# Performance work log

Hardware: AMD Instinct MI355X
Metric: run time of the kernel (lower is better)

The kernel has to match this reference:

```python
import jax, jax.numpy as jnp
import numpy as np

EPS = 1e-5
TOP_K = 2


def setup_inputs() -> dict:
    key = jax.random.key(0)
    ks = jax.random.split(key, 8)
    B, T, D, E, F = 4, 2048, 1024, 8, 4096
    s_in = 1.0 / np.sqrt(D)
    s_ff = 1.0 / np.sqrt(F)
    return {
        "hidden_states": jax.random.normal(ks[0], (B, T, D), jnp.float32),
        "input_tensor": jax.random.normal(ks[1], (B, T, D), jnp.float32),
        "gate_w": jax.random.normal(ks[2], (D, E), jnp.float32) * s_in,
        "gate_b": jnp.zeros((E,), jnp.float32),
        "w1": jax.random.normal(ks[3], (E, D, F), jnp.float32) * s_in,
        "b1": jnp.zeros((E, F), jnp.float32),
        "w2": jax.random.normal(ks[4], (E, F, D), jnp.float32) * s_ff,
        "b2": jnp.zeros((E, D), jnp.float32),
        "gamma": jnp.ones((D,), jnp.float32),
        "beta": jnp.zeros((D,), jnp.float32),
    }


def _layer_norm(x, gamma, beta):
    mu = jnp.mean(x, axis=-1, keepdims=True)
    var = jnp.mean(jnp.square(x - mu), axis=-1, keepdims=True)
    return (x - mu) * jax.lax.rsqrt(var + EPS) * gamma + beta


def reference(hidden_states, input_tensor, gate_w, gate_b, w1, b1, w2, b2, gamma, beta):
    E = gate_b.shape[0]
    # Router: softmax over experts, then top-k gate values/indices.
    gate_logits = jnp.einsum("btd,de->bte", hidden_states, gate_w) + gate_b
    gate_probs = jax.nn.softmax(gate_logits, axis=-1)
    topk_gates, topk_idx = jax.lax.top_k(gate_probs, TOP_K)  # [B,T,K]
    # Combine weights per expert: sum of top-k gate values routed to expert e.
    combine_w = jnp.sum(
        jax.nn.one_hot(topk_idx, E, dtype=hidden_states.dtype)
        * topk_gates[..., None],
        axis=-2,
    )  # [B,T,E]
    # Dispatch/combine: weighted sum of expert FFN outputs (loop over small fixed E).
    expert_outputs = jnp.zeros_like(hidden_states)
    for e in range(E):
        h = jax.nn.gelu(jnp.einsum("btd,df->btf", hidden_states, w1[e]) + b1[e])
        y = jnp.einsum("btf,fd->btd", h, w2[e]) + b2[e]
        expert_outputs = expert_outputs + combine_w[..., e:e + 1] * y
    # Dropout is identity in eval mode.
    return _layer_norm(expert_outputs + input_tensor, gamma, beta)
```

## Files before the change

kernel.cpp:

```cpp
#include <hip/hip_runtime.h>

#define TOKENS 8192
#define DIM 1024
#define NEXP 8
#define FDIM 4096

typedef __bf16 bf16x8 __attribute__((ext_vector_type(8)));
typedef float f32x4 __attribute__((ext_vector_type(4)));
typedef float f32x16 __attribute__((ext_vector_type(16)));

__device__ __forceinline__ unsigned short f2bf(float f) {
  unsigned u = __builtin_bit_cast(unsigned, f);
  u += 0x7fffu + ((u >> 16) & 1u);
  return (unsigned short)(u >> 16);
}

__device__ __forceinline__ float bf2f(unsigned short s) {
  unsigned u = (unsigned)s << 16;
  return __builtin_bit_cast(float, u);
}

__device__ __forceinline__ void gload16(const void* g, void* l) {
  __builtin_amdgcn_global_load_lds(
      (const __attribute__((address_space(1))) unsigned int*)g,
      (__attribute__((address_space(3))) unsigned int*)l, 16, 0, 0);
}

__device__ __forceinline__ void transpose_tile(const float* __restrict__ src,
                                               unsigned short* __restrict__ dstp,
                                               int R, int C, int bi2,
                                               void* smraw, int tid) {
  unsigned int (*lt)[64] = (unsigned int(*)[64])smraw;
  const int e = bi2 >> 9;
  const int w = bi2 & 511;
  const int nft = C >> 6;
  const int dt = w / nft, ft = w % nft;
  const int r0 = dt * 128, c0 = ft * 64;
  const float* s = src + (size_t)e * R * C;
  unsigned short* dout = dstp + (size_t)e * R * C;

#pragma unroll
  for (int pi = 0; pi < 4; ++pi) {
    const int idx = tid + pi * 256;
    const int dp = idx >> 4;
    const int f0 = (idx & 15) * 4;
    const float4 va = *(const float4*)(s + (size_t)(r0 + dp * 2) * C + c0 + f0);
    const float4 vb = *(const float4*)(s + (size_t)(r0 + dp * 2 + 1) * C + c0 + f0);
    const float a[4] = {va.x, va.y, va.z, va.w};
    const float b[4] = {vb.x, vb.y, vb.z, vb.w};
#pragma unroll
    for (int j = 0; j < 4; ++j) {
      const int f = f0 + j;
      lt[f][dp ^ (((f >> 2) & 7) << 2)] =
          (unsigned)f2bf(a[j]) | ((unsigned)f2bf(b[j]) << 16);
    }
  }
  __syncthreads();
#pragma unroll
  for (int wi = 0; wi < 4; ++wi) {
    const int idx = tid + wi * 256;
    const int f = idx >> 4;
    const int dp0 = (idx & 15) * 4;
    const int sw = ((f >> 2) & 7) << 2;
    uint4 o = *(const uint4*)&lt[f][dp0 ^ sw];
    *(uint4*)(dout + (size_t)(c0 + f) * R + r0 + dp0 * 2) = o;
  }
}

__global__ void prep_kernel(const float* __restrict__ w1,
                            unsigned short* __restrict__ w1t,
                            const float* __restrict__ hs,
                            const float* __restrict__ gw,
                            const float* __restrict__ gb,
                            int* __restrict__ counts,
                            int* __restrict__ tok_idx,
                            float* __restrict__ tok_w,
                            unsigned int* __restrict__ slotinfo,
                            unsigned short* __restrict__ hs_bf) {
  __shared__ unsigned int lt[64][64];
  const int L = blockIdx.x;

  if (L < 2048) {
    const int lane = threadIdx.x & 63;
    const int wid = threadIdx.x >> 6;
    const int t = L * 4 + wid;
    const float* row = hs + (size_t)t * DIM;

    float x[16];
    const float4* r4 = (const float4*)(row + lane * 16);
#pragma unroll
    for (int i = 0; i < 4; ++i) {
      float4 v = r4[i];
      x[i * 4 + 0] = v.x; x[i * 4 + 1] = v.y; x[i * 4 + 2] = v.z; x[i * 4 + 3] = v.w;
    }

    float acc[8];
#pragma unroll
    for (int e = 0; e < 8; ++e) acc[e] = 0.f;
#pragma unroll
    for (int i = 0; i < 16; ++i) {
      const int d = lane * 16 + i;
      const float4* g4 = (const float4*)(gw + (size_t)d * 8);
      float4 g0 = g4[0], g1 = g4[1];
      const float xv = x[i];
      acc[0] += xv * g0.x; acc[1] += xv * g0.y; acc[2] += xv * g0.z; acc[3] += xv * g0.w;
      acc[4] += xv * g1.x; acc[5] += xv * g1.y; acc[6] += xv * g1.z; acc[7] += xv * g1.w;
    }
#pragma unroll
    for (int sh = 1; sh < 64; sh <<= 1) {
#pragma unroll
      for (int e = 0; e < 8; ++e) acc[e] += __shfl_xor(acc[e], sh, 64);
    }
#pragma unroll
    for (int e = 0; e < 8; ++e) acc[e] += gb[e];

    float mx = acc[0];
#pragma unroll
    for (int e = 1; e < 8; ++e) mx = fmaxf(mx, acc[e]);
    float p[8];
    float sum = 0.f;
#pragma unroll
    for (int e = 0; e < 8; ++e) { p[e] = __expf(acc[e] - mx); sum += p[e]; }
    const float inv = 1.0f / sum;

    int i0 = 0; float b0 = p[0];
#pragma unroll
    for (int e = 1; e < 8; ++e) if (p[e] > b0) { b0 = p[e]; i0 = e; }
    int i1 = -1; float b1v = -1.f;
#pragma unroll
    for (int e = 0; e < 8; ++e) if (e != i0 && p[e] > b1v) { b1v = p[e]; i1 = e; }

    if (lane == 0) {
      int pos0 = atomicAdd(&counts[i0], 1);
      tok_idx[i0 * TOKENS + pos0] = t;
      tok_w[i0 * TOKENS + pos0] = b0 * inv;
      int pos1 = atomicAdd(&counts[i1], 1);
      tok_idx[i1 * TOKENS + pos1] = t;
      tok_w[i1 * TOKENS + pos1] = b1v * inv;
      slotinfo[t] = ((unsigned)i0 << 29) | ((unsigned)pos0 << 16) |
                    ((unsigned)i1 << 13) | (unsigned)pos1;
    }

    unsigned short us[16];
#pragma unroll
    for (int i = 0; i < 16; ++i) us[i] = f2bf(x[i]);
    uint4 o0, o1;
    o0.x = (unsigned)us[0] | ((unsigned)us[1] << 16);
    o0.y = (unsigned)us[2] | ((unsigned)us[3] << 16);
    o0.z = (unsigned)us[4] | ((unsigned)us[5] << 16);
    o0.w = (unsigned)us[6] | ((unsigned)us[7] << 16);
    o1.x = (unsigned)us[8] | ((unsigned)us[9] << 16);
    o1.y = (unsigned)us[10] | ((unsigned)us[11] << 16);
    o1.z = (unsigned)us[12] | ((unsigned)us[13] << 16);
    o1.w = (unsigned)us[14] | ((unsigned)us[15] << 16);
    uint4* dst = (uint4*)(hs_bf + (size_t)t * DIM + lane * 16);
    dst[0] = o0;
    dst[1] = o1;
    return;
  }

  transpose_tile(w1, w1t, DIM, FDIM, L - 2048, lt, threadIdx.x);
}

template<int MODE, int K, int N>
__global__ __launch_bounds__(256, 4)
void moe_gemm(const unsigned short* __restrict__ Abase,
              const unsigned short* __restrict__ Bbase,
              const float* __restrict__ bias,
              const int* __restrict__ counts,
              const int* __restrict__ tok_idx,
              unsigned short* __restrict__ dst,
              const float* __restrict__ w2src,
              unsigned short* __restrict__ w2t) {
  constexpr int NS = K / 32;
  constexpr int NQ = (MODE == 0) ? 8 : 2;
  __shared__ __align__(16) unsigned char sm[32768];

  int L = blockIdx.x;
  if (MODE == 0) {
    const int q = L / 5, r = L % 5;
    if (r >= 3) {
      transpose_tile(w2src, w2t, FDIM, DIM, q * 2 + (r - 3), sm, threadIdx.x);
      return;
    }
    L = q * 3 + r;
  }

  const int xk = L & 7;
  const int tt = L >> 3;
  const int g = (tt >> 4) * 8 + xk;
  const int within = tt & 15;

  int e = 0, mcq = 0, n4 = 0, goff = 0, cnt = 0;
  {
    int accC = 0, accOff = 0;
    bool found = false;
#pragma unroll
    for (int ee = 0; ee < NEXP; ++ee) {
      const int c = counts[ee];
      const int mt = (c + 127) >> 7;
      const int mc4 = (mt + 3) >> 2;
      const int ch = mc4 * NQ;
      if (!found && g < accC + ch) {
        const int local = g - accC;
        e = ee;
        mcq = (local / NQ) * 4;
        n4 = (local % NQ) * 4;
        goff = accOff;
        cnt = c;
        found = true;
      }
      accC += ch;
      accOff += c;
    }
    if (!found) return;
  }
  const int m0 = (mcq + (within >> 2)) * 128;
  if (m0 >= cnt) return;
  const int n0 = (n4 + (within & 3)) * 128;

  const int tid = threadIdx.x;
  const int lane = tid & 63;
  const int wid = tid >> 6;
  const int wm = wid >> 1;
  const int wn = wid & 1;
  const int l31 = lane & 31;
  const int lh = lane >> 5;

  const int trow = tid >> 2;
  const int tswz = (tid & 3) ^ ((trow >> 1) & 3) ^ ((trow >> 3) & 3);
  const unsigned char* Bexp = (const unsigned char*)(Bbase + (size_t)e * K * N);

  int gA0 = m0 + trow;      if (gA0 > cnt - 1) gA0 = cnt - 1;
  int gA1 = m0 + trow + 64; if (gA1 > cnt - 1) gA1 = cnt - 1;
  size_t rowA0, rowA1;
  if (MODE == 0) {
    rowA0 = (size_t)tok_idx[e * TOKENS + gA0] * K;
    rowA1 = (size_t)tok_idx[e * TOKENS + gA1] * K;
  } else {
    rowA0 = (size_t)(goff + gA0) * K;
    rowA1 = (size_t)(goff + gA1) * K;
  }
  const unsigned char* pA0 = (const unsigned char*)(Abase + rowA0) + tswz * 16;
  const unsigned char* pA1 = (const unsigned char*)(Abase + rowA1) + tswz * 16;
  const unsigned char* pB0 = Bexp + (size_t)(n0 + trow) * (K * 2) + tswz * 16;
  const unsigned char* pB1 = Bexp + (size_t)(n0 + trow + 64) * (K * 2) + tswz * 16;

  const int sw = ((l31 >> 1) & 3) ^ ((l31 >> 3) & 3);
  const int cE = lh ^ sw;
  const int aB = wm * 4096 + l31 * 64 + cE * 16;
  const int bB = 8192 + wn * 4096 + l31 * 64 + cE * 16;
  const unsigned char* smc = (const unsigned char*)sm;
  unsigned char* smw = (unsigned char*)sm + tid * 16;

  f32x16 acc[2][2];
#pragma unroll
  for (int mb = 0; mb < 2; ++mb)
#pragma unroll
    for (int nb = 0; nb < 2; ++nb)
#pragma unroll
      for (int r = 0; r < 16; ++r) acc[mb][nb][r] = 0.f;

  gload16(pA0, smw);
  gload16(pA1, smw + 4096);
  gload16(pB0, smw + 8192);
  gload16(pB1, smw + 12288);
  pA0 += 64; pA1 += 64; pB0 += 64; pB1 += 64;

#pragma unroll 1
  for (int st = 0; st < NS; ++st) {
    const int cs = (st & 1) << 14;
    const int ns = ((st + 1) & 1) << 14;
    if (st < NS - 1) {
      gload16(pA0, smw + ns);
      gload16(pA1, smw + ns + 4096);
      gload16(pB0, smw + ns + 8192);
      gload16(pB1, smw + ns + 12288);
      pA0 += 64; pA1 += 64; pB0 += 64; pB1 += 64;
      asm volatile("s_waitcnt vmcnt(4)" ::: "memory");
    } else {
      asm volatile("s_waitcnt vmcnt(0)" ::: "memory");
    }
    __builtin_amdgcn_s_barrier();
    __builtin_amdgcn_sched_barrier(0);
#pragma unroll
    for (int kq = 0; kq < 2; ++kq) {
      const int ko = kq << 5;
      bf16x8 a0 = *(const bf16x8*)(smc + cs + (aB ^ ko));
      bf16x8 a1 = *(const bf16x8*)(smc + cs + ((aB + 2048) ^ ko));
      bf16x8 b0 = *(const bf16x8*)(smc + cs + (bB ^ ko));
      bf16x8 b1 = *(const bf16x8*)(smc + cs + ((bB + 2048) ^ ko));
      acc[0][0] = __builtin_amdgcn_mfma_f32_32x32x16_bf16(a0, b0, acc[0][0], 0, 0, 0);
      acc[0][1] = __builtin_amdgcn_mfma_f32_32x32x16_bf16(a0, b1, acc[0][1], 0, 0, 0);
      acc[1][0] = __builtin_amdgcn_mfma_f32_32x32x16_bf16(a1, b0, acc[1][0], 0, 0, 0);
      acc[1][1] = __builtin_amdgcn_mfma_f32_32x32x16_bf16(a1, b1, acc[1][1], 0, 0, 0);
    }
    __builtin_amdgcn_sched_barrier(0);
    asm volatile("s_waitcnt lgkmcnt(0)" ::: "memory");
    __builtin_amdgcn_s_barrier();
  }

#pragma unroll
  for (int nb = 0; nb < 2; ++nb) {
    const int fcol = n0 + wn * 64 + nb * 32 + l31;
    const float bv = bias[e * N + fcol];
#pragma unroll
    for (int mb = 0; mb < 2; ++mb) {
#pragma unroll
      for (int r = 0; r < 16; ++r) {
        const int ml = wm * 64 + mb * 32 + (r & 3) + 8 * (r >> 2) + 4 * lh;
        const int gm = m0 + ml;
        if (gm < cnt) {
          float v = acc[mb][nb][r] + bv;
          if (MODE == 0) {
            const float u = 0.7978845608028654f * (v + 0.044715f * v * v * v);
            const float th = 1.0f - 2.0f / (1.0f + __expf(2.0f * u));
            v = 0.5f * v * (1.0f + th);
          }
          dst[(size_t)(goff + gm) * N + fcol] = f2bf(v);
        }
      }
    }
  }
}

__global__ void ln_combine_kernel(const unsigned short* __restrict__ y_buf,
                                  const float* __restrict__ in_t,
                                  const int* __restrict__ counts,
                                  const unsigned int* __restrict__ slotinfo,
                                  const float* __restrict__ tok_w,
                                  const float* __restrict__ gamma,
                                  const float* __restrict__ beta,
                                  float* __restrict__ out) {
  const int lane = threadIdx.x & 63;
  const int wid = threadIdx.x >> 6;
  const int t = blockIdx.x * 4 + wid;

  const unsigned s = slotinfo[t];
  const int e0 = s >> 29, p0 = (s >> 16) & 8191;
  const int e1 = (s >> 13) & 7, p1 = s & 8191;
  int off0 = 0, off1 = 0;
#pragma unroll
  for (int ee = 0; ee < NEXP; ++ee) {
    const int c = counts[ee];
    if (ee < e0) off0 += c;
    if (ee < e1) off1 += c;
  }
  const float w0 = tok_w[e0 * TOKENS + p0];
  const float w1 = tok_w[e1 * TOKENS + p1];
  const size_t r0 = (size_t)(off0 + p0) * DIM;
  const size_t r1 = (size_t)(off1 + p1) * DIM;

  float v[16];
  {
    const float4* i4 = (const float4*)(in_t + (size_t)t * DIM + lane * 16);
    const uint4* y0 = (const uint4*)(y_buf + r0 + lane * 16);
    const uint4* y1 = (const uint4*)(y_buf + r1 + lane * 16);
#pragma unroll
    for (int i = 0; i < 4; ++i) {
      float4 a = i4[i];
      v[i * 4 + 0] = a.x; v[i * 4 + 1] = a.y; v[i * 4 + 2] = a.z; v[i * 4 + 3] = a.w;
    }
#pragma unroll
    for (int i = 0; i < 2; ++i) {
      uint4 u0 = y0[i];
      uint4 u1 = y1[i];
      const unsigned uw0[4] = {u0.x, u0.y, u0.z, u0.w};
      const unsigned uw1[4] = {u1.x, u1.y, u1.z, u1.w};
#pragma unroll
      for (int k = 0; k < 4; ++k) {
        const int base = i * 8 + k * 2;
        v[base + 0] += w0 * bf2f((unsigned short)(uw0[k] & 0xffff)) +
                       w1 * bf2f((unsigned short)(uw1[k] & 0xffff));
        v[base + 1] += w0 * bf2f((unsigned short)(uw0[k] >> 16)) +
                       w1 * bf2f((unsigned short)(uw1[k] >> 16));
      }
    }
  }

  float sum = 0.f, s2 = 0.f;
#pragma unroll
  for (int i = 0; i < 16; ++i) { sum += v[i]; s2 += v[i] * v[i]; }
#pragma unroll
  for (int sh = 1; sh < 64; sh <<= 1) {
    sum += __shfl_xor(sum, sh, 64);
    s2 += __shfl_xor(s2, sh, 64);
  }
  const float mu = sum * (1.0f / DIM);
  const float var = s2 * (1.0f / DIM) - mu * mu;
  const float rs = rsqrtf(var + 1e-5f);

  float4* w4 = (float4*)(out + (size_t)t * DIM + lane * 16);
#pragma unroll
  for (int i = 0; i < 4; ++i) {
    const int d = lane * 16 + i * 4;
    float4 gg = *(const float4*)(gamma + d);
    float4 bb = *(const float4*)(beta + d);
    float4 o;
    o.x = (v[i * 4 + 0] - mu) * rs * gg.x + bb.x;
    o.y = (v[i * 4 + 1] - mu) * rs * gg.y + bb.y;
    o.z = (v[i * 4 + 2] - mu) * rs * gg.z + bb.z;
    o.w = (v[i * 4 + 3] - mu) * rs * gg.w + bb.w;
    w4[i] = o;
  }
}

extern "C" void kernel_launch(void* const* d_in, const int* in_sizes, int n_in,
                              void* d_out, int out_size, void* d_ws, size_t ws_size,
                              hipStream_t stream) {
  const float* hs    = (const float*)d_in[0];
  const float* in_t  = (const float*)d_in[1];
  const float* gw    = (const float*)d_in[2];
  const float* gb    = (const float*)d_in[3];
  const float* w1    = (const float*)d_in[4];
  const float* b1    = (const float*)d_in[5];
  const float* w2    = (const float*)d_in[6];
  const float* b2    = (const float*)d_in[7];
  const float* gamma = (const float*)d_in[8];
  const float* beta  = (const float*)d_in[9];
  float* out = (float*)d_out;
  char* ws = (char*)d_ws;

  int* counts            = (int*)(ws + 0);
  unsigned int* slotinfo = (unsigned int*)(ws + 512);
  int* tok_idx           = (int*)(ws + 66048);
  float* tok_w           = (float*)(ws + 328192);
  unsigned short* hs_bf  = (unsigned short*)(ws + 590336);
  unsigned short* w1t    = (unsigned short*)(ws + 17367552);
  unsigned short* w2t    = (unsigned short*)(ws + 84476416);
  unsigned short* h_buf  = (unsigned short*)(ws + 151585280);
  unsigned short* y_buf  = (unsigned short*)(ws + 590336);

  hipMemsetAsync(counts, 0, NEXP * sizeof(int), stream);
  prep_kernel<<<6144, 256, 0, stream>>>(w1, w1t, hs, gw, gb, counts, tok_idx,
                                        tok_w, slotinfo, hs_bf);
  moe_gemm<0, DIM, FDIM><<<10240, 256, 0, stream>>>(
      hs_bf, w1t, b1, counts, tok_idx, h_buf, w2, w2t);
  moe_gemm<1, FDIM, DIM><<<2048, 256, 0, stream>>>(
      h_buf, w2t, b2, counts, tok_idx, y_buf, nullptr, nullptr);
  ln_combine_kernel<<<TOKENS / 4, 256, 0, stream>>>(y_buf, in_t, counts, slotinfo,
                                                    tok_w, gamma, beta, out);
}
```

Measured before the change: 709.5 us.

## Fuse w1 fp32-to-bf16 transpose into first expert GEMM B-tile loading

```diff
diff --git a/kernel.cpp b/kernel.cpp
--- a/kernel.cpp
+++ b/kernel.cpp
@@ -67,9 +67,7 @@
   }
 }
 
-__global__ void prep_kernel(const float* __restrict__ w1,
-                            unsigned short* __restrict__ w1t,
-                            const float* __restrict__ hs,
+__global__ void prep_kernel(const float* __restrict__ hs,
                             const float* __restrict__ gw,
                             const float* __restrict__ gb,
                             int* __restrict__ counts,
@@ -77,101 +75,94 @@
                             float* __restrict__ tok_w,
                             unsigned int* __restrict__ slotinfo,
                             unsigned short* __restrict__ hs_bf) {
-  __shared__ unsigned int lt[64][64];
-  const int L = blockIdx.x;
-
-  if (L < 2048) {
-    const int lane = threadIdx.x & 63;
-    const int wid = threadIdx.x >> 6;
-    const int t = L * 4 + wid;
-    const float* row = hs + (size_t)t * DIM;
-
-    float x[16];
-    const float4* r4 = (const float4*)(row + lane * 16);
-#pragma unroll
-    for (int i = 0; i < 4; ++i) {
-      float4 v = r4[i];
-      x[i * 4 + 0] = v.x; x[i * 4 + 1] = v.y; x[i * 4 + 2] = v.z; x[i * 4 + 3] = v.w;
-    }
-
-    float acc[8];
-#pragma unroll
-    for (int e = 0; e < 8; ++e) acc[e] = 0.f;
-#pragma unroll
-    for (int i = 0; i < 16; ++i) {
-      const int d = lane * 16 + i;
-      const float4* g4 = (const float4*)(gw + (size_t)d * 8);
-      float4 g0 = g4[0], g1 = g4[1];
-      const float xv = x[i];
-      acc[0] += xv * g0.x; acc[1] += xv * g0.y; acc[2] += xv * g0.z; acc[3] += xv * g0.w;
-      acc[4] += xv * g1.x; acc[5] += xv * g1.y; acc[6] += xv * g1.z; acc[7] += xv * g1.w;
-    }
-#pragma unroll
-    for (int sh = 1; sh < 64; sh <<= 1) {
-#pragma unroll
-      for (int e = 0; e < 8; ++e) acc[e] += __shfl_xor(acc[e], sh, 64);
-    }
-#pragma unroll
-    for (int e = 0; e < 8; ++e) acc[e] += gb[e];
-
-    float mx = acc[0];
-#pragma unroll
-    for (int e = 1; e < 8; ++e) mx = fmaxf(mx, acc[e]);
-    float p[8];
-    float sum = 0.f;
-#pragma unroll
-    for (int e = 0; e < 8; ++e) { p[e] = __expf(acc[e] - mx); sum += p[e]; }
-    const float inv = 1.0f / sum;
-
-    int i0 = 0; float b0 = p[0];
-#pragma unroll
-    for (int e = 1; e < 8; ++e) if (p[e] > b0) { b0 = p[e]; i0 = e; }
-    int i1 = -1; float b1v = -1.f;
-#pragma unroll
-    for (int e = 0; e < 8; ++e) if (e != i0 && p[e] > b1v) { b1v = p[e]; i1 = e; }
-
-    if (lane == 0) {
-      int pos0 = atomicAdd(&counts[i0], 1);
-      tok_idx[i0 * TOKENS + pos0] = t;
-      tok_w[i0 * TOKENS + pos0] = b0 * inv;
-      int pos1 = atomicAdd(&counts[i1], 1);
-      tok_idx[i1 * TOKENS + pos1] = t;
-      tok_w[i1 * TOKENS + pos1] = b1v * inv;
-      slotinfo[t] = ((unsigned)i0 << 29) | ((unsigned)pos0 << 16) |
-                    ((unsigned)i1 << 13) | (unsigned)pos1;
-    }
-
-    unsigned short us[16];
-#pragma unroll
-    for (int i = 0; i < 16; ++i) us[i] = f2bf(x[i]);
-    uint4 o0, o1;
-    o0.x = (unsigned)us[0] | ((unsigned)us[1] << 16);
-    o0.y = (unsigned)us[2] | ((unsigned)us[3] << 16);
-    o0.z = (unsigned)us[4] | ((unsigned)us[5] << 16);
-    o0.w = (unsigned)us[6] | ((unsigned)us[7] << 16);
-    o1.x = (unsigned)us[8] | ((unsigned)us[9] << 16);
-    o1.y = (unsigned)us[10] | ((unsigned)us[11] << 16);
-    o1.z = (unsigned)us[12] | ((unsigned)us[13] << 16);
-    o1.w = (unsigned)us[14] | ((unsigned)us[15] << 16);
-    uint4* dst = (uint4*)(hs_bf + (size_t)t * DIM + lane * 16);
-    dst[0] = o0;
-    dst[1] = o1;
-    return;
-  }
-
-  transpose_tile(w1, w1t, DIM, FDIM, L - 2048, lt, threadIdx.x);
+  const int lane = threadIdx.x & 63;
+  const int wid = threadIdx.x >> 6;
+  const int t = blockIdx.x * 4 + wid;
+  const float* row = hs + (size_t)t * DIM;
+
+  float x[16];
+  const float4* r4 = (const float4*)(row + lane * 16);
+#pragma unroll
+  for (int i = 0; i < 4; ++i) {
+    float4 v = r4[i];
+    x[i * 4 + 0] = v.x; x[i * 4 + 1] = v.y; x[i * 4 + 2] = v.z; x[i * 4 + 3] = v.w;
+  }
+
+  float acc[8];
+#pragma unroll
+  for (int e = 0; e < 8; ++e) acc[e] = 0.f;
+#pragma unroll
+  for (int i = 0; i < 16; ++i) {
+    const int d = lane * 16 + i;
+    const float4* g4 = (const float4*)(gw + (size_t)d * 8);
+    float4 g0 = g4[0], g1 = g4[1];
+    const float xv = x[i];
+    acc[0] += xv * g0.x; acc[1] += xv * g0.y; acc[2] += xv * g0.z; acc[3] += xv * g0.w;
+    acc[4] += xv * g1.x; acc[5] += xv * g1.y; acc[6] += xv * g1.z; acc[7] += xv * g1.w;
+  }
+#pragma unroll
+  for (int sh = 1; sh < 64; sh <<= 1) {
+#pragma unroll
+    for (int e = 0; e < 8; ++e) acc[e] += __shfl_xor(acc[e], sh, 64);
+  }
+#pragma unroll
+  for (int e = 0; e < 8; ++e) acc[e] += gb[e];
+
+  float mx = acc[0];
+#pragma unroll
+  for (int e = 1; e < 8; ++e) mx = fmaxf(mx, acc[e]);
+  float p[8];
+  float sum = 0.f;
+#pragma unroll
+  for (int e = 0; e < 8; ++e) { p[e] = __expf(acc[e] - mx); sum += p[e]; }
+  const float inv = 1.0f / sum;
+
+  int i0 = 0; float b0 = p[0];
+#pragma unroll
+  for (int e = 1; e < 8; ++e) if (p[e] > b0) { b0 = p[e]; i0 = e; }
+  int i1 = -1; float b1v = -1.f;
+#pragma unroll
+  for (int e = 0; e < 8; ++e) if (e != i0 && p[e] > b1v) { b1v = p[e]; i1 = e; }
+
+  if (lane == 0) {
+    int pos0 = atomicAdd(&counts[i0], 1);
+    tok_idx[i0 * TOKENS + pos0] = t;
+    tok_w[i0 * TOKENS + pos0] = b0 * inv;
+    int pos1 = atomicAdd(&counts[i1], 1);
+    tok_idx[i1 * TOKENS + pos1] = t;
+    tok_w[i1 * TOKENS + pos1] = b1v * inv;
+    slotinfo[t] = ((unsigned)i0 << 29) | ((unsigned)pos0 << 16) |
+                  ((unsigned)i1 << 13) | (unsigned)pos1;
+  }
+
+  unsigned short us[16];
+#pragma unroll
+  for (int i = 0; i < 16; ++i) us[i] = f2bf(x[i]);
+  uint4 o0, o1;
+  o0.x = (unsigned)us[0] | ((unsigned)us[1] << 16);
+  o0.y = (unsigned)us[2] | ((unsigned)us[3] << 16);
+  o0.z = (unsigned)us[4] | ((unsigned)us[5] << 16);
+  o0.w = (unsigned)us[6] | ((unsigned)us[7] << 16);
+  o1.x = (unsigned)us[8] | ((unsigned)us[9] << 16);
+  o1.y = (unsigned)us[10] | ((unsigned)us[11] << 16);
+  o1.z = (unsigned)us[12] | ((unsigned)us[13] << 16);
+  o1.w = (unsigned)us[14] | ((unsigned)us[15] << 16);
+  uint4* dst = (uint4*)(hs_bf + (size_t)t * DIM + lane * 16);
+  dst[0] = o0;
+  dst[1] = o1;
 }
 
 template<int MODE, int K, int N>
 __global__ __launch_bounds__(256, 4)
 void moe_gemm(const unsigned short* __restrict__ Abase,
               const unsigned short* __restrict__ Bbase,
+              const float* __restrict__ B32,
               const float* __restrict__ bias,
               const int* __restrict__ counts,
               const int* __restrict__ tok_idx,
               unsigned short* __restrict__ dst,
-              const float* __restrict__ w2src,
-              unsigned short* __restrict__ w2t) {
+              const float* __restrict__ fsrc,
+              unsigned short* __restrict__ fdst) {
   constexpr int NS = K / 32;
   constexpr int NQ = (MODE == 0) ? 8 : 2;
   __shared__ __align__(16) unsigned char sm[32768];
@@ -180,7 +171,7 @@
   if (MODE == 0) {
     const int q = L / 5, r = L % 5;
     if (r >= 3) {
-      transpose_tile(w2src, w2t, FDIM, DIM, q * 2 + (r - 3), sm, threadIdx.x);
+      transpose_tile(fsrc, fdst, FDIM, DIM, q * 2 + (r - 3), sm, threadIdx.x);
       return;
     }
     L = q * 3 + r;
@@ -229,7 +220,6 @@
 
   const int trow = tid >> 2;
   const int tswz = (tid & 3) ^ ((trow >> 1) & 3) ^ ((trow >> 3) & 3);
-  const unsigned char* Bexp = (const unsigned char*)(Bbase + (size_t)e * K * N);
 
   int gA0 = m0 + trow;      if (gA0 > cnt - 1) gA0 = cnt - 1;
   int gA1 = m0 + trow + 64; if (gA1 > cnt - 1) gA1 = cnt - 1;
@@ -243,8 +233,22 @@
   }
   const unsigned char* pA0 = (const unsigned char*)(Abase + rowA0) + tswz * 16;
   const unsigned char* pA1 = (const unsigned char*)(Abase + rowA1) + tswz * 16;
-  const unsigned char* pB0 = Bexp + (size_t)(n0 + trow) * (K * 2) + tswz * 16;
-  const unsigned char* pB1 = Bexp + (size_t)(n0 + trow + 64) * (K * 2) + tswz * 16;
+
+  const unsigned char* pB0 = nullptr;
+  const unsigned char* pB1 = nullptr;
+  const float* pB32a = nullptr;
+  const float* pB32b = nullptr;
+  const int kp = tid & 15;
+  const int c4a = tid >> 4;
+  if (MODE == 1) {
+    const unsigned char* Bexp = (const unsigned char*)(Bbase + (size_t)e * K * N);
+    pB0 = Bexp + (size_t)(n0 + trow) * (K * 2) + tswz * 16;
+    pB1 = Bexp + (size_t)(n0 + trow + 64) * (K * 2) + tswz * 16;
+  } else {
+    const float* w1e = B32 + (size_t)e * K * N;
+    pB32a = w1e + (size_t)(2 * kp) * N + n0 + 4 * c4a;
+    pB32b = pB32a + N;
+  }
 
   const int sw = ((l31 >> 1) & 3) ^ ((l31 >> 3) & 3);
   const int cE = lh ^ sw;
@@ -261,11 +265,40 @@
 #pragma unroll
       for (int r = 0; r < 16; ++r) acc[mb][nb][r] = 0.f;
 
+  float4 ra0, rb0, ra1, rb1;
+
+  auto bwrite = [&](unsigned char* bw, int c4, float4 a, float4 b) {
+    const float av[4] = {a.x, a.y, a.z, a.w};
+    const float bv[4] = {b.x, b.y, b.z, b.w};
+    const int o = kp >> 2;
+    const int lo = kp & 3;
+#pragma unroll
+    for (int j = 0; j < 4; ++j) {
+      const int r = c4 * 4 + j;
+      const int s = ((r >> 1) & 3) ^ ((r >> 3) & 3);
+      *(unsigned*)(bw + r * 64 + (((o ^ s) << 2) | lo) * 4) =
+          (unsigned)f2bf(av[j]) | ((unsigned)f2bf(bv[j]) << 16);
+    }
+  };
+
   gload16(pA0, smw);
   gload16(pA1, smw + 4096);
-  gload16(pB0, smw + 8192);
-  gload16(pB1, smw + 12288);
-  pA0 += 64; pA1 += 64; pB0 += 64; pB1 += 64;
+  if (MODE == 1) {
+    gload16(pB0, smw + 8192);
+    gload16(pB1, smw + 12288);
+    pB0 += 64; pB1 += 64;
+  } else {
+    ra0 = *(const float4*)pB32a;
+    rb0 = *(const float4*)pB32b;
+    ra1 = *(const float4*)(pB32a + 64);
+    rb1 = *(const float4*)(pB32b + 64);
+    pB32a += 32 * N; pB32b += 32 * N;
+    bwrite((unsigned char*)sm + 8192, c4a, ra0, rb0);
+    bwrite((unsigned char*)sm + 8192, c4a + 16, ra1, rb1);
+  }
+  pA0 += 64; pA1 += 64;
+  asm volatile("s_waitcnt vmcnt(0) lgkmcnt(0)" ::: "memory");
+  __builtin_amdgcn_s_barrier();
 
 #pragma unroll 1
   for (int st = 0; st < NS; ++st) {
@@ -274,14 +307,25 @@
     if (st < NS - 1) {
       gload16(pA0, smw + ns);
       gload16(pA1, smw + ns + 4096);
-      gload16(pB0, smw + ns + 8192);
-      gload16(pB1, smw + ns + 12288);
-      pA0 += 64; pA1 += 64; pB0 += 64; pB1 += 64;
-      asm volatile("s_waitcnt vmcnt(4)" ::: "memory");
-    } else {
+      pA0 += 64; pA1 += 64;
+      if (MODE == 1) {
+        gload16(pB0, smw + ns + 8192);
+        gload16(pB1, smw + ns + 12288);
+        pB0 += 64; pB1 += 64;
+        asm volatile("s_waitcnt vmcnt(4)" ::: "memory");
+      } else {
+        ra0 = *(const float4*)pB32a;
+        rb0 = *(const float4*)pB32b;
+        ra1 = *(const float4*)(pB32a + 64);
+        rb1 = *(const float4*)(pB32b + 64);
+        pB32a += 32 * N; pB32b += 32 * N;
+      }
+    } else if (MODE == 1) {
       asm volatile("s_waitcnt vmcnt(0)" ::: "memory");
     }
-    __builtin_amdgcn_s_barrier();
+    if (MODE == 1) {
+      __builtin_amdgcn_s_barrier();
+    }
     __builtin_amdgcn_sched_barrier(0);
 #pragma unroll
     for (int kq = 0; kq < 2; ++kq) {
@@ -296,6 +340,11 @@
       acc[1][1] = __builtin_amdgcn_mfma_f32_32x32x16_bf16(a1, b1, acc[1][1], 0, 0, 0);
     }
     __builtin_amdgcn_sched_barrier(0);
+    if (MODE == 0 && st < NS - 1) {
+      bwrite((unsigned char*)sm + ns + 8192, c4a, ra0, rb0);
+      bwrite((unsigned char*)sm + ns + 8192, c4a + 16, ra1, rb1);
+      __builtin_amdgcn_sched_barrier(0);
+    }
     asm volatile("s_waitcnt lgkmcnt(0)" ::: "memory");
     __builtin_amdgcn_s_barrier();
   }
@@ -426,18 +475,17 @@
   int* tok_idx           = (int*)(ws + 66048);
   float* tok_w           = (float*)(ws + 328192);
   unsigned short* hs_bf  = (unsigned short*)(ws + 590336);
-  unsigned short* w1t    = (unsigned short*)(ws + 17367552);
   unsigned short* w2t    = (unsigned short*)(ws + 84476416);
   unsigned short* h_buf  = (unsigned short*)(ws + 151585280);
   unsigned short* y_buf  = (unsigned short*)(ws + 590336);
 
   hipMemsetAsync(counts, 0, NEXP * sizeof(int), stream);
-  prep_kernel<<<6144, 256, 0, stream>>>(w1, w1t, hs, gw, gb, counts, tok_idx,
+  prep_kernel<<<2048, 256, 0, stream>>>(hs, gw, gb, counts, tok_idx,
                                         tok_w, slotinfo, hs_bf);
   moe_gemm<0, DIM, FDIM><<<10240, 256, 0, stream>>>(
-      hs_bf, w1t, b1, counts, tok_idx, h_buf, w2, w2t);
+      hs_bf, nullptr, w1, b1, counts, tok_idx, h_buf, w2, w2t);
   moe_gemm<1, FDIM, DIM><<<2048, 256, 0, stream>>>(
-      h_buf, w2t, b2, counts, tok_idx, y_buf, nullptr, nullptr);
+      h_buf, w2t, nullptr, b2, counts, tok_idx, y_buf, nullptr, nullptr);
   ln_combine_kernel<<<TOKENS / 4, 256, 0, stream>>>(y_buf, in_t, counts, slotinfo,
                                                     tok_w, gamma, beta, out);
 }
```

After: 833.8 us. 17.5% more time.
